# Kernel optimization log

Measured on AMD Instinct MI355X. Metric: run time of the kernel, lower is better.

## Reference

```python
import jax, jax.numpy as jnp
import numpy as np


def setup_inputs() -> dict:
    key = jax.random.key(0)
    k1, k2 = jax.random.split(key)
    N, I, J, K = 256, 32, 32, 256
    x = jax.random.normal(k1, (N, I, K), dtype=jnp.float32)
    z = jax.random.normal(k2, (N, J, K), dtype=jnp.float32)
    return {"x": x, "z": z}


def reference(x, z):
    # Original torch code loops over batch rolls; rolling only permutes the set
    # over which log_softmax (a permutation-invariant logsumexp) is taken, and
    # index 0 of the roll stack is always the diagonal pair (x[n], z[n]).
    # So it is exactly a symmetric InfoNCE over the full pairwise score matrix.
    J = z.shape[1]
    # Full pairwise token-level similarity: [N_x, N_z, I, J]
    sim = jnp.einsum('aik,bjk->abij', x, z)
    # score(x_a, z_b) = sum_{i,j} softmax_i(sim)*sim / J
    w = jax.nn.softmax(sim, axis=2) * sim
    S = w.sum(axis=(2, 3)) / J  # [N_x, N_z]
    diag = jnp.diagonal(S)
    # loss_x[n] = -log_softmax over x-candidates (axis 0) at the diagonal
    loss_x = jax.nn.logsumexp(S, axis=0) - diag
    # loss_z[n] = -log_softmax over z-candidates (axis 1) at the diagonal
    loss_z = jax.nn.logsumexp(S, axis=1) - diag
    loss = loss_x + loss_z
    return loss.mean()  # reduction='mean'
```

## Files before the change

kernel.cpp:

```cpp
#include <hip/hip_runtime.h>
#include <hip/hip_bf16.h>
#include <stdint.h>


typedef __attribute__((ext_vector_type(8))) short short8;
typedef __attribute__((ext_vector_type(16))) float float16;

#define NTOK 256
#define KDIM 256

__device__ __forceinline__ unsigned short f2bf(float f) {
    unsigned int u = __float_as_uint(f);
    unsigned int r = (u + 0x7fffu + ((u >> 16) & 1u)) >> 16;
    return (unsigned short)r;
}

__device__ __forceinline__ short8 cvt8(const float* p) {
    float4 f0 = ((const float4*)p)[0];
    float4 f1 = ((const float4*)p)[1];
    short8 v;
    v[0] = (short)f2bf(f0.x); v[1] = (short)f2bf(f0.y);
    v[2] = (short)f2bf(f0.z); v[3] = (short)f2bf(f0.w);
    v[4] = (short)f2bf(f1.x); v[5] = (short)f2bf(f1.y);
    v[6] = (short)f2bf(f1.z); v[7] = (short)f2bf(f1.w);
    return v;
}

__global__ void conv_kernel(const float* __restrict__ x,
                            const float* __restrict__ z,
                            short8* __restrict__ outbf,
                            float* __restrict__ out0) {
    const int uid = blockIdx.x * 256 + threadIdx.x;
    if (uid == 0) out0[0] = 0.0f;
    const int u = uid & 262143;
    const float* src = (uid < 262144) ? x : z;
    const int g  = u >> 10;
    const int r  = u & 1023;
    const int ks = r >> 6;
    const int h  = (r >> 5) & 1;
    const int l  = r & 31;
    outbf[uid] = cvt8(src + ((g * 32 + l) * KDIM + ks * 16 + h * 8));
}

__device__ __forceinline__ void tile_epilogue(const float16& c, float* S,
                                              int a, int b, int lane) {
    float m8[8], m4[4];
#pragma unroll
    for (int r = 0; r < 8; r++) m8[r] = fmaxf(c[2 * r], c[2 * r + 1]);
#pragma unroll
    for (int r = 0; r < 4; r++) m4[r] = fmaxf(m8[2 * r], m8[2 * r + 1]);
    float m = fmaxf(fmaxf(m4[0], m4[1]), fmaxf(m4[2], m4[3]));
    m = fmaxf(m, __shfl_xor(m, 32, 64));

    float e[16];
#pragma unroll
    for (int r = 0; r < 16; r++) e[r] = __expf(c[r] - m);

    float s8[8], s4[4];
#pragma unroll
    for (int r = 0; r < 8; r++) s8[r] = e[2 * r] + e[2 * r + 1];
#pragma unroll
    for (int r = 0; r < 4; r++) s4[r] = s8[2 * r] + s8[2 * r + 1];
    float se = (s4[0] + s4[1]) + (s4[2] + s4[3]);

    float w8[8], w4[4];
#pragma unroll
    for (int r = 0; r < 8; r++)
        w8[r] = fmaf(e[2 * r + 1], c[2 * r + 1], e[2 * r] * c[2 * r]);
#pragma unroll
    for (int r = 0; r < 4; r++) w4[r] = w8[2 * r] + w8[2 * r + 1];
    float swe = (w4[0] + w4[1]) + (w4[2] + w4[3]);

    se  += __shfl_xor(se, 32, 64);
    swe += __shfl_xor(swe, 32, 64);
    float cv = swe * __builtin_amdgcn_rcpf(se);
#pragma unroll
    for (int off = 1; off < 32; off <<= 1) cv += __shfl_xor(cv, off, 64);
    if (lane == 0) S[a * NTOK + b] = cv * (1.0f / 32.0f);
}

template <bool F32SRC>
__global__ __launch_bounds__(256, 2)
void sim_kernel(const short8* __restrict__ xbf, const short8* __restrict__ zbf,
                const float* __restrict__ xf, const float* __restrict__ zf,
                float* __restrict__ S) {
    const int tid  = threadIdx.x;
    const int lane = tid & 63;
    const int wid  = tid >> 6;
    const int l31  = lane & 31;
    const int half = lane >> 5;
    const int bid  = blockIdx.x;

    const int ap  = (bid >> 4) * 4 + wid;
    const int ag0 = ap * 2;
    const int ag1 = ap * 2 + 1;
    const int bg0 = (bid & 15) * 16;

    short8 A0[16], A1[16];
    if (F32SRC) {
        const float* fa0 = xf + ((ag0 * 32 + l31) * KDIM + half * 8);
        const float* fa1 = xf + ((ag1 * 32 + l31) * KDIM + half * 8);
#pragma unroll
        for (int k = 0; k < 16; k++) {
            A0[k] = cvt8(fa0 + k * 16);
            A1[k] = cvt8(fa1 + k * 16);
        }
    } else {
        const short8* pa = xbf + ag0 * 1024 + lane;
#pragma unroll
        for (int k = 0; k < 16; k++) {
            A0[k] = pa[k * 64];
            A1[k] = pa[1024 + k * 64];
        }
    }

#pragma unroll 1
    for (int bi = 0; bi < 16; bi++) {
        const int bg = bg0 + bi;
        short8 B[16];
        if (F32SRC) {
            const float* fb = zf + ((bg * 32 + l31) * KDIM + half * 8);
#pragma unroll
            for (int k = 0; k < 16; k++) B[k] = cvt8(fb + k * 16);
        } else {
            const short8* pb = zbf + bg * 1024 + lane;
#pragma unroll
            for (int k = 0; k < 16; k++) B[k] = pb[k * 64];
        }

        float16 acc0, acc1;
#pragma unroll
        for (int r = 0; r < 16; r++) { acc0[r] = 0.0f; acc1[r] = 0.0f; }
#pragma unroll
        for (int k = 0; k < 16; k++) {
            acc0 = __builtin_amdgcn_mfma_f32_32x32x16_bf16(A0[k], B[k], acc0, 0, 0, 0);
            acc1 = __builtin_amdgcn_mfma_f32_32x32x16_bf16(A1[k], B[k], acc1, 0, 0, 0);
        }

        tile_epilogue(acc0, S, ag0, bg, lane);
        tile_epilogue(acc1, S, ag1, bg, lane);
    }
}

__global__ void loss_part(const float* __restrict__ S, float* __restrict__ out) {
    const int lane = threadIdx.x & 63;
    const int wid  = threadIdx.x >> 6;
    const int n    = blockIdx.x * 4 + wid;

    float cv[4], rv[4];
#pragma unroll
    for (int k = 0; k < 4; k++) {
        const int t = lane + 64 * k;
        cv[k] = S[t * NTOK + n];
        rv[k] = S[n * NTOK + t];
    }
    float m = fmaxf(fmaxf(cv[0], cv[1]), fmaxf(cv[2], cv[3]));
#pragma unroll
    for (int off = 1; off < 64; off <<= 1) m = fmaxf(m, __shfl_xor(m, off, 64));
    float s = 0.0f;
#pragma unroll
    for (int k = 0; k < 4; k++) s += __expf(cv[k] - m);
#pragma unroll
    for (int off = 1; off < 64; off <<= 1) s += __shfl_xor(s, off, 64);
    float lse_col = m + __logf(s);

    float m2 = fmaxf(fmaxf(rv[0], rv[1]), fmaxf(rv[2], rv[3]));
#pragma unroll
    for (int off = 1; off < 64; off <<= 1) m2 = fmaxf(m2, __shfl_xor(m2, off, 64));
    float s2 = 0.0f;
#pragma unroll
    for (int k = 0; k < 4; k++) s2 += __expf(rv[k] - m2);
#pragma unroll
    for (int off = 1; off < 64; off <<= 1) s2 += __shfl_xor(s2, off, 64);
    float lse_row = m2 + __logf(s2);

    __shared__ float red[4];
    if (lane == 0) {
        float diag = S[n * NTOK + n];
        red[wid] = (lse_col - diag) + (lse_row - diag);
    }
    __syncthreads();
    if (threadIdx.x == 0)
        atomicAdd(out, (red[0] + red[1] + red[2] + red[3]) * (1.0f / 256.0f));
}

__global__ void zero_kernel(float* __restrict__ out) {
    out[0] = 0.0f;
}

extern "C" void kernel_launch(void* const* d_in, const int* in_sizes, int n_in,
                              void* d_out, int out_size, void* d_ws, size_t ws_size,
                              hipStream_t stream) {
    const float* x = (const float*)d_in[0];
    const float* z = (const float*)d_in[1];
    float* out = (float*)d_out;

    const size_t bf_bytes = 524288ull * 16ull;
    const size_t s_bytes  = 256ull * 256ull * 4ull;

    if (ws_size >= bf_bytes + s_bytes) {
        short8* xbf = (short8*)d_ws;
        short8* zbf = xbf + 262144;
        float*  S   = (float*)((char*)d_ws + bf_bytes);
        conv_kernel<<<2048, 256, 0, stream>>>(x, z, (short8*)d_ws, out);
        sim_kernel<false><<<512, 256, 0, stream>>>(xbf, zbf, nullptr, nullptr, S);
        loss_part<<<64, 256, 0, stream>>>(S, out);
    } else {
        float* S = (float*)d_ws;
        zero_kernel<<<1, 1, 0, stream>>>(out);
        sim_kernel<true><<<512, 256, 0, stream>>>(nullptr, nullptr, x, z, S);
        loss_part<<<64, 256, 0, stream>>>(S, out);
    }
}
```

Before: 118.2 us.

## Stage shared z tiles through double-buffered LDS via global_load_lds

In the bf16 path, each block's four waves now copy each z tile cooperatively into LDS with direct global-to-LDS loads, double buffered so the next tile's load overlaps the current MFMA work. Before this, every wave loaded the full B tile from global memory into its own registers. The change is meant to cut redundant global traffic and hide load latency. It adds a barrier per iteration and 32 KB of LDS per block, which may limit occupancy. The fp32 fallback path is split off and now converts each B fragment inline rather than loading the whole tile into registers first.

```diff
diff --git a/kernel.cpp b/kernel.cpp
--- a/kernel.cpp
+++ b/kernel.cpp
@@ -5,6 +5,9 @@
 
 typedef __attribute__((ext_vector_type(8))) short short8;
 typedef __attribute__((ext_vector_type(16))) float float16;
+
+typedef const __attribute__((address_space(1))) unsigned int* gptr_as1;
+typedef __attribute__((address_space(3))) unsigned int* lptr_as3;
 
 #define NTOK 256
 #define KDIM 256
@@ -84,6 +87,8 @@
 void sim_kernel(const short8* __restrict__ xbf, const short8* __restrict__ zbf,
                 const float* __restrict__ xf, const float* __restrict__ zf,
                 float* __restrict__ S) {
+    __shared__ short8 smem[2048];
+
     const int tid  = threadIdx.x;
     const int lane = tid & 63;
     const int wid  = tid >> 6;
@@ -113,33 +118,69 @@
             A1[k] = pa[1024 + k * 64];
         }
     }
+#pragma unroll
+    for (int k = 0; k < 16; k++) {
+        asm volatile("" : "+v"(A0[k]));
+        asm volatile("" : "+v"(A1[k]));
+    }
+
+    if (F32SRC) {
+#pragma unroll 1
+        for (int bi = 0; bi < 16; bi++) {
+            const int bg = bg0 + bi;
+            const float* fb = zf + ((bg * 32 + l31) * KDIM + half * 8);
+            float16 acc0, acc1;
+#pragma unroll
+            for (int r = 0; r < 16; r++) { acc0[r] = 0.0f; acc1[r] = 0.0f; }
+#pragma unroll
+            for (int k = 0; k < 16; k++) {
+                short8 B = cvt8(fb + k * 16);
+                acc0 = __builtin_amdgcn_mfma_f32_32x32x16_bf16(A0[k], B, acc0, 0, 0, 0);
+                acc1 = __builtin_amdgcn_mfma_f32_32x32x16_bf16(A1[k], B, acc1, 0, 0, 0);
+            }
+            tile_epilogue(acc0, S, ag0, bg, lane);
+            tile_epilogue(acc1, S, ag1, bg, lane);
+        }
+        return;
+    }
+
+    const short8* zsl = zbf + (size_t)bg0 * 1024;
+#define STAGE(buf, bi)                                                        \
+    {                                                                         \
+        const short8* gsrc = zsl + (bi) * 1024 + wid * 256 + lane;            \
+        short8* ldst = &smem[(buf) * 1024 + wid * 256];                       \
+        __builtin_amdgcn_global_load_lds((gptr_as1)(gsrc),       (lptr_as3)(ldst),       16, 0, 0); \
+        __builtin_amdgcn_global_load_lds((gptr_as1)(gsrc + 64),  (lptr_as3)(ldst + 64),  16, 0, 0); \
+        __builtin_amdgcn_global_load_lds((gptr_as1)(gsrc + 128), (lptr_as3)(ldst + 128), 16, 0, 0); \
+        __builtin_amdgcn_global_load_lds((gptr_as1)(gsrc + 192), (lptr_as3)(ldst + 192), 16, 0, 0); \
+    }
+
+    STAGE(0, 0);
+    __syncthreads();
 
 #pragma unroll 1
     for (int bi = 0; bi < 16; bi++) {
+        const int cur = bi & 1;
+        if (bi + 1 < 16) STAGE(1 - cur, bi + 1);
+
+        const short8* lb = &smem[cur * 1024];
+        float16 acc0, acc1;
+#pragma unroll
+        for (int r = 0; r < 16; r++) { acc0[r] = 0.0f; acc1[r] = 0.0f; }
+#pragma unroll
+        for (int k = 0; k < 16; k++) {
+            short8 B = lb[k * 64 + lane];
+            acc0 = __builtin_amdgcn_mfma_f32_32x32x16_bf16(A0[k], B, acc0, 0, 0, 0);
+            acc1 = __builtin_amdgcn_mfma_f32_32x32x16_bf16(A1[k], B, acc1, 0, 0, 0);
+        }
+
         const int bg = bg0 + bi;
-        short8 B[16];
-        if (F32SRC) {
-            const float* fb = zf + ((bg * 32 + l31) * KDIM + half * 8);
-#pragma unroll
-            for (int k = 0; k < 16; k++) B[k] = cvt8(fb + k * 16);
-        } else {
-            const short8* pb = zbf + bg * 1024 + lane;
-#pragma unroll
-            for (int k = 0; k < 16; k++) B[k] = pb[k * 64];
-        }
-
-        float16 acc0, acc1;
-#pragma unroll
-        for (int r = 0; r < 16; r++) { acc0[r] = 0.0f; acc1[r] = 0.0f; }
-#pragma unroll
-        for (int k = 0; k < 16; k++) {
-            acc0 = __builtin_amdgcn_mfma_f32_32x32x16_bf16(A0[k], B[k], acc0, 0, 0, 0);
-            acc1 = __builtin_amdgcn_mfma_f32_32x32x16_bf16(A1[k], B[k], acc1, 0, 0, 0);
-        }
-
         tile_epilogue(acc0, S, ag0, bg, lane);
         tile_epilogue(acc1, S, ag1, bg, lane);
-    }
+
+        __syncthreads();
+    }
+#undef STAGE
 }
 
 __global__ void loss_part(const float* __restrict__ S, float* __restrict__ out) {
```

Measured after the change: 113.5 us. -4.0%, faster.

## Share A tile via LDS and compute 2x2 MFMA tiles per wave

Applied to the files above, without the earlier changes.

Each block now loads a pair of x batches into LDS once with direct global-to-LDS loads, and its four waves share that tile. Each wave computes a 2x2 block of (a,b) score tiles per iteration, so every A and B fragment is reused twice. A and B are no longer held in large register arrays, the grid doubles to 1024 blocks and the occupancy hint rises to 3. The epilogue is rewritten as a single fused pass over exp, sum and weighted sum with four accumulators. This trades register-resident A for LDS reads and adds a block-wide sync.

```diff
diff --git a/kernel.cpp b/kernel.cpp
--- a/kernel.cpp
+++ b/kernel.cpp
@@ -5,6 +5,9 @@
 
 typedef __attribute__((ext_vector_type(8))) short short8;
 typedef __attribute__((ext_vector_type(16))) float float16;
+
+typedef const __attribute__((address_space(1))) unsigned int* gptr_as1;
+typedef __attribute__((address_space(3))) unsigned int* lptr_as3;
 
 #define NTOK 256
 #define KDIM 256
@@ -42,7 +45,7 @@
     outbf[uid] = cvt8(src + ((g * 32 + l) * KDIM + ks * 16 + h * 8));
 }
 
-__device__ __forceinline__ void tile_epilogue(const float16& c, float* S,
+__device__ __forceinline__ void tile_epilogue(const float16& c, float* __restrict__ S,
                                               int a, int b, int lane) {
     float m8[8], m4[4];
 #pragma unroll
@@ -52,24 +55,22 @@
     float m = fmaxf(fmaxf(m4[0], m4[1]), fmaxf(m4[2], m4[3]));
     m = fmaxf(m, __shfl_xor(m, 32, 64));
 
-    float e[16];
-#pragma unroll
-    for (int r = 0; r < 16; r++) e[r] = __expf(c[r] - m);
-
-    float s8[8], s4[4];
-#pragma unroll
-    for (int r = 0; r < 8; r++) s8[r] = e[2 * r] + e[2 * r + 1];
-#pragma unroll
-    for (int r = 0; r < 4; r++) s4[r] = s8[2 * r] + s8[2 * r + 1];
-    float se = (s4[0] + s4[1]) + (s4[2] + s4[3]);
-
-    float w8[8], w4[4];
-#pragma unroll
-    for (int r = 0; r < 8; r++)
-        w8[r] = fmaf(e[2 * r + 1], c[2 * r + 1], e[2 * r] * c[2 * r]);
-#pragma unroll
-    for (int r = 0; r < 4; r++) w4[r] = w8[2 * r] + w8[2 * r + 1];
-    float swe = (w4[0] + w4[1]) + (w4[2] + w4[3]);
+    float s0 = 0.f, s1 = 0.f, s2 = 0.f, s3 = 0.f;
+    float w0 = 0.f, w1 = 0.f, w2 = 0.f, w3 = 0.f;
+#pragma unroll
+    for (int r = 0; r < 16; r += 4) {
+        float e0 = __expf(c[r + 0] - m);
+        float e1 = __expf(c[r + 1] - m);
+        float e2 = __expf(c[r + 2] - m);
+        float e3 = __expf(c[r + 3] - m);
+        s0 += e0; s1 += e1; s2 += e2; s3 += e3;
+        w0 = fmaf(e0, c[r + 0], w0);
+        w1 = fmaf(e1, c[r + 1], w1);
+        w2 = fmaf(e2, c[r + 2], w2);
+        w3 = fmaf(e3, c[r + 3], w3);
+    }
+    float se  = (s0 + s1) + (s2 + s3);
+    float swe = (w0 + w1) + (w2 + w3);
 
     se  += __shfl_xor(se, 32, 64);
     swe += __shfl_xor(swe, 32, 64);
@@ -80,65 +81,80 @@
 }
 
 template <bool F32SRC>
-__global__ __launch_bounds__(256, 2)
+__global__ __launch_bounds__(256, 3)
 void sim_kernel(const short8* __restrict__ xbf, const short8* __restrict__ zbf,
                 const float* __restrict__ xf, const float* __restrict__ zf,
                 float* __restrict__ S) {
+    __shared__ short8 sA[2048];
+
     const int tid  = threadIdx.x;
     const int lane = tid & 63;
-    const int wid  = tid >> 6;
+    const int w    = tid >> 6;
     const int l31  = lane & 31;
     const int half = lane >> 5;
-    const int bid  = blockIdx.x;
-
-    const int ap  = (bid >> 4) * 4 + wid;
-    const int ag0 = ap * 2;
-    const int ag1 = ap * 2 + 1;
-    const int bg0 = (bid & 15) * 16;
-
-    short8 A0[16], A1[16];
-    if (F32SRC) {
-        const float* fa0 = xf + ((ag0 * 32 + l31) * KDIM + half * 8);
-        const float* fa1 = xf + ((ag1 * 32 + l31) * KDIM + half * 8);
-#pragma unroll
-        for (int k = 0; k < 16; k++) {
-            A0[k] = cvt8(fa0 + k * 16);
-            A1[k] = cvt8(fa1 + k * 16);
+
+    const int apair = blockIdx.x >> 3;
+    const int ag0   = apair * 2, ag1 = ag0 + 1;
+    const int bbase = (blockIdx.x & 7) * 32 + w * 8;
+
+    if (!F32SRC) {
+        const short8* asrc = xbf + apair * 2048;
+#pragma unroll
+        for (int i = 0; i < 8; i++) {
+            const short8* g = asrc + i * 256 + w * 64 + lane;
+            short8* l = &sA[i * 256 + w * 64];
+            __builtin_amdgcn_global_load_lds((gptr_as1)g, (lptr_as3)l, 16, 0, 0);
         }
-    } else {
-        const short8* pa = xbf + ag0 * 1024 + lane;
-#pragma unroll
-        for (int k = 0; k < 16; k++) {
-            A0[k] = pa[k * 64];
-            A1[k] = pa[1024 + k * 64];
+        __syncthreads();
+    }
+
+#pragma unroll 1
+    for (int p = 0; p < 4; p++) {
+        const int bgA = bbase + 2 * p;
+        const int bgB = bgA + 1;
+
+        float16 acc00, acc01, acc10, acc11;
+#pragma unroll
+        for (int r = 0; r < 16; r++) {
+            acc00[r] = 0.f; acc01[r] = 0.f; acc10[r] = 0.f; acc11[r] = 0.f;
         }
-    }
-
-#pragma unroll 1
-    for (int bi = 0; bi < 16; bi++) {
-        const int bg = bg0 + bi;
-        short8 B[16];
+
         if (F32SRC) {
-            const float* fb = zf + ((bg * 32 + l31) * KDIM + half * 8);
-#pragma unroll
-            for (int k = 0; k < 16; k++) B[k] = cvt8(fb + k * 16);
+            const float* fa0 = xf + ((ag0 * 32 + l31) * KDIM + half * 8);
+            const float* fa1 = xf + ((ag1 * 32 + l31) * KDIM + half * 8);
+            const float* fba = zf + ((bgA * 32 + l31) * KDIM + half * 8);
+            const float* fbb = zf + ((bgB * 32 + l31) * KDIM + half * 8);
+#pragma unroll
+            for (int ks = 0; ks < 16; ks++) {
+                short8 A0 = cvt8(fa0 + ks * 16);
+                short8 A1 = cvt8(fa1 + ks * 16);
+                short8 Ba = cvt8(fba + ks * 16);
+                short8 Bb = cvt8(fbb + ks * 16);
+                acc00 = __builtin_amdgcn_mfma_f32_32x32x16_bf16(A0, Ba, acc00, 0, 0, 0);
+                acc01 = __builtin_amdgcn_mfma_f32_32x32x16_bf16(A0, Bb, acc01, 0, 0, 0);
+                acc10 = __builtin_amdgcn_mfma_f32_32x32x16_bf16(A1, Ba, acc10, 0, 0, 0);
+                acc11 = __builtin_amdgcn_mfma_f32_32x32x16_bf16(A1, Bb, acc11, 0, 0, 0);
+            }
         } else {
-            const short8* pb = zbf + bg * 1024 + lane;
-#pragma unroll
-            for (int k = 0; k < 16; k++) B[k] = pb[k * 64];
+            const short8* pba = zbf + bgA * 1024 + lane;
+            const short8* pbb = zbf + bgB * 1024 + lane;
+#pragma unroll
+            for (int ks = 0; ks < 16; ks++) {
+                short8 Ba = pba[ks * 64];
+                short8 Bb = pbb[ks * 64];
+                short8 A0 = sA[ks * 64 + lane];
+                short8 A1 = sA[1024 + ks * 64 + lane];
+                acc00 = __builtin_amdgcn_mfma_f32_32x32x16_bf16(A0, Ba, acc00, 0, 0, 0);
+                acc01 = __builtin_amdgcn_mfma_f32_32x32x16_bf16(A0, Bb, acc01, 0, 0, 0);
+                acc10 = __builtin_amdgcn_mfma_f32_32x32x16_bf16(A1, Ba, acc10, 0, 0, 0);
+                acc11 = __builtin_amdgcn_mfma_f32_32x32x16_bf16(A1, Bb, acc11, 0, 0, 0);
+            }
         }
 
-        float16 acc0, acc1;
-#pragma unroll
-        for (int r = 0; r < 16; r++) { acc0[r] = 0.0f; acc1[r] = 0.0f; }
-#pragma unroll
-        for (int k = 0; k < 16; k++) {
-            acc0 = __builtin_amdgcn_mfma_f32_32x32x16_bf16(A0[k], B[k], acc0, 0, 0, 0);
-            acc1 = __builtin_amdgcn_mfma_f32_32x32x16_bf16(A1[k], B[k], acc1, 0, 0, 0);
-        }
-
-        tile_epilogue(acc0, S, ag0, bg, lane);
-        tile_epilogue(acc1, S, ag1, bg, lane);
+        tile_epilogue(acc00, S, ag0, bgA, lane);
+        tile_epilogue(acc01, S, ag0, bgB, lane);
+        tile_epilogue(acc10, S, ag1, bgA, lane);
+        tile_epilogue(acc11, S, ag1, bgB, lane);
     }
 }
 
@@ -203,12 +219,12 @@
         short8* zbf = xbf + 262144;
         float*  S   = (float*)((char*)d_ws + bf_bytes);
         conv_kernel<<<2048, 256, 0, stream>>>(x, z, (short8*)d_ws, out);
-        sim_kernel<false><<<512, 256, 0, stream>>>(xbf, zbf, nullptr, nullptr, S);
+        sim_kernel<false><<<1024, 256, 0, stream>>>(xbf, zbf, nullptr, nullptr, S);
         loss_part<<<64, 256, 0, stream>>>(S, out);
     } else {
         float* S = (float*)d_ws;
         zero_kernel<<<1, 1, 0, stream>>>(out);
-        sim_kernel<true><<<512, 256, 0, stream>>>(nullptr, nullptr, x, z, S);
+        sim_kernel<true><<<1024, 256, 0, stream>>>(nullptr, nullptr, x, z, S);
         loss_part<<<64, 256, 0, stream>>>(S, out);
     }
 }
```

Result: slower. 179.6 us (+51.9%).
